# Kernel optimization log

Measured on AMD Instinct MI355X. Metric: run time of the kernel, lower is better.

## Reference

```python
import jax, jax.numpy as jnp
import numpy as np

B, S, E = 2, 2048, 1024
H = 16
A = 1024
DH = A // H  # 64 per-head attention dim


def setup_inputs() -> dict:
    key = jax.random.key(0)
    ks = jax.random.split(key, 9)
    s = lambda fan_in: 1.0 / np.sqrt(fan_in)
    return {
        "x": jax.random.normal(ks[0], (B, S, E), dtype=jnp.float32),
        # per-head Q/K/V projections stacked over heads: [H, E, DH]
        "Wq": jax.random.normal(ks[1], (H, E, DH), dtype=jnp.float32) * s(E),
        "bq": jnp.zeros((H, DH), dtype=jnp.float32),
        "Wk": jax.random.normal(ks[2], (H, E, DH), dtype=jnp.float32) * s(E),
        "bk": jnp.zeros((H, DH), dtype=jnp.float32),
        "Wv": jax.random.normal(ks[3], (H, E, DH), dtype=jnp.float32) * s(E),
        "bv": jnp.zeros((H, DH), dtype=jnp.float32),
        # output projection Linear(A, E): stored as [A, E]
        "Wo": jax.random.normal(ks[4], (A, E), dtype=jnp.float32) * s(A),
        "bo": jnp.zeros((E,), dtype=jnp.float32),
    }


def reference(x, Wq, bq, Wk, bk, Wv, bv, Wo, bo):
    # Batched equivalent of the per-head Python loop:
    # each head: q = x Wq_h + bq_h ; scores = q k^T / sqrt(DH) ; softmax ; @ v
    q = jnp.einsum("bse,hed->bhsd", x, Wq) + bq[None, :, None, :]
    k = jnp.einsum("bse,hed->bhsd", x, Wk) + bk[None, :, None, :]
    v = jnp.einsum("bse,hed->bhsd", x, Wv) + bv[None, :, None, :]
    scale = 1.0 / jnp.sqrt(jnp.asarray(DH, dtype=x.dtype))
    scores = jnp.einsum("bhsd,bhtd->bhst", q, k) * scale  # [B,H,S,S]
    attn = jax.nn.softmax(scores, axis=-1)
    heads = jnp.einsum("bhst,bhtd->bhsd", attn, v)  # [B,H,S,DH]
    # concat heads along last dim (matches torch.cat over head outputs)
    concat = heads.transpose(0, 2, 1, 3).reshape(x.shape[0], x.shape[1], H * DH)
    return concat @ Wo + bo  # final Linear(dim_attention, dim_embedding)
```

## Files before the change

kernel.cpp:

```cpp
#include <hip/hip_runtime.h>
#include <math.h>


namespace {
constexpr int kBn = 2, kS = 2048, kE = 1024, kH = 16, kDH = 64, kA = 1024;

typedef __attribute__((ext_vector_type(8))) short short8;
typedef __attribute__((ext_vector_type(4))) float f32x4;

#define QSCALE 0.18033688011112042f

__device__ inline unsigned short f2bf(float f) {
  union { float f; unsigned u; } x; x.f = f;
  unsigned r = x.u + 0x7fffu + ((x.u >> 16) & 1u);
  return (unsigned short)(r >> 16);
}

__device__ inline void gld16(const void* g, void* l) {
  __builtin_amdgcn_global_load_lds(
      (const __attribute__((address_space(1))) unsigned int*)g,
      (__attribute__((address_space(3))) unsigned int*)l, 16, 0, 0);
}

__global__ __launch_bounds__(256) void cast_x_kernel(
    const float* __restrict__ x, unsigned short* __restrict__ xb) {
  const int i = (blockIdx.x * 256 + threadIdx.x) * 8;
  float4 a = *(const float4*)(x + i);
  float4 b = *(const float4*)(x + i + 4);
  unsigned short t[8];
  t[0] = f2bf(a.x); t[1] = f2bf(a.y); t[2] = f2bf(a.z); t[3] = f2bf(a.w);
  t[4] = f2bf(b.x); t[5] = f2bf(b.y); t[6] = f2bf(b.z); t[7] = f2bf(b.w);
  *(short8*)(xb + i) = *(const short8*)t;
}

__global__ __launch_bounds__(256) void cast_wqkv_kernel(
    const float* __restrict__ Wq, const float* __restrict__ Wk,
    const float* __restrict__ Wv, unsigned short* __restrict__ Wt) {
  const int sel = blockIdx.z;
  const float* __restrict__ W = (sel == 0) ? Wq : (sel == 1) ? Wk : Wv;
  const int h = blockIdx.y;
  const int e0 = blockIdx.x * 64;
  const int tid = threadIdx.x;

  __shared__ float T[64][68];
  const int el = tid >> 2, dq = tid & 3;
  const float* src = W + ((size_t)h * kE + e0 + el) * kDH + dq * 16;
#pragma unroll
  for (int j = 0; j < 4; ++j)
    *(float4*)&T[el][dq * 16 + j * 4] = *(const float4*)(src + j * 4);
  __syncthreads();

  const int d = tid & 63, w = tid >> 6;
  unsigned short t[16];
#pragma unroll
  for (int j = 0; j < 16; ++j) t[j] = f2bf(T[w * 16 + j][d]);
  unsigned short* dst =
      Wt + (((size_t)sel << 20) | ((size_t)(h * 64 + d) << 10)) + e0 + w * 16;
  *(short8*)dst = *(const short8*)&t[0];
  *(short8*)(dst + 8) = *(const short8*)&t[8];
}

__global__ __launch_bounds__(256) void cast_wo_kernel(
    const float* __restrict__ Wo, unsigned short* __restrict__ Wot) {
  const int a0 = blockIdx.x * 64, e0 = blockIdx.y * 64;
  const int tid = threadIdx.x;

  __shared__ float T[64][68];
  const int al = tid >> 2, dq = tid & 3;
  const float* src = Wo + (size_t)(a0 + al) * kE + e0 + dq * 16;
#pragma unroll
  for (int j = 0; j < 4; ++j)
    *(float4*)&T[al][dq * 16 + j * 4] = *(const float4*)(src + j * 4);
  __syncthreads();

  const int e = tid & 63, w = tid >> 6;
  unsigned short t[16];
#pragma unroll
  for (int j = 0; j < 16; ++j) t[j] = f2bf(T[w * 16 + j][e]);
  unsigned short* dst = Wot + ((size_t)(e0 + e) << 10) + a0 + w * 16;
  *(short8*)dst = *(const short8*)&t[0];
  *(short8*)(dst + 8) = *(const short8*)&t[8];
}

__global__ __launch_bounds__(256) void gemm_bf16_kernel(
    const unsigned short* __restrict__ A, const unsigned short* __restrict__ Bt,
    const float* __restrict__ b0, const float* __restrict__ b1,
    const float* __restrict__ b2,
    unsigned short* __restrict__ oq, unsigned short* __restrict__ okk,
    unsigned short* __restrict__ ov, float* __restrict__ of, int modeBase) {
  constexpr int K = 1024;
  const int mode = modeBase ? 3 : (int)blockIdx.z;
  const unsigned short* Bm = Bt + ((size_t)(modeBase ? 0 : blockIdx.z) << 20);
  const float* bias = (mode == 1) ? b1 : (mode == 2) ? b2 : b0;

  const int mt = blockIdx.x, nt = blockIdx.y;
  const int tid = threadIdx.x;
  const int wv = tid >> 6, lane = tid & 63, lq = lane & 15, quad = lane >> 4;
  const int wm = wv >> 1, wn = wv & 1;

  __shared__ unsigned short lA[128 * 32];
  __shared__ unsigned short lB[128 * 32];

  const int c0 = wv * 64 + lane;
  const int c1 = c0 + 256;
  const unsigned short* gA0 = A + (size_t)(mt * 128 + (c0 >> 2)) * K + (c0 & 3) * 8;
  const unsigned short* gA1 = A + (size_t)(mt * 128 + (c1 >> 2)) * K + (c1 & 3) * 8;
  const unsigned short* gB0 = Bm + (size_t)(nt * 128 + (c0 >> 2)) * K + (c0 & 3) * 8;
  const unsigned short* gB1 = Bm + (size_t)(nt * 128 + (c1 >> 2)) * K + (c1 & 3) * 8;
  unsigned short* lA0 = lA + (size_t)(wv * 64) * 8;
  unsigned short* lA1 = lA0 + 256 * 8;
  unsigned short* lB0 = lB + (size_t)(wv * 64) * 8;
  unsigned short* lB1 = lB0 + 256 * 8;

  f32x4 acc[4][4];
#pragma unroll
  for (int i = 0; i < 4; ++i)
#pragma unroll
    for (int j = 0; j < 4; ++j) acc[i][j] = (f32x4){0.f, 0.f, 0.f, 0.f};

  for (int k0 = 0; k0 < K; k0 += 32) {
    gld16(gA0 + k0, lA0);
    gld16(gA1 + k0, lA1);
    gld16(gB0 + k0, lB0);
    gld16(gB1 + k0, lB1);
    __syncthreads();
    short8 af[4], bfr[4];
#pragma unroll
    for (int i = 0; i < 4; ++i)
      af[i] = *(const short8*)&lA[(wm * 64 + i * 16 + lq) * 32 + quad * 8];
#pragma unroll
    for (int j = 0; j < 4; ++j)
      bfr[j] = *(const short8*)&lB[(wn * 64 + j * 16 + lq) * 32 + quad * 8];
#pragma unroll
    for (int i = 0; i < 4; ++i)
#pragma unroll
      for (int j = 0; j < 4; ++j)
        acc[i][j] = __builtin_amdgcn_mfma_f32_16x16x32_bf16(af[i], bfr[j],
                                                            acc[i][j], 0, 0, 0);
    __syncthreads();
  }

  const int n0 = nt * 128 + wn * 64;
  float bv4[4];
#pragma unroll
  for (int j = 0; j < 4; ++j) bv4[j] = bias[n0 + j * 16 + lq];

  if (mode == 3) {
    const int m0 = mt * 128 + wm * 64;
#pragma unroll
    for (int i = 0; i < 4; ++i)
#pragma unroll
      for (int j = 0; j < 4; ++j)
#pragma unroll
        for (int r = 0; r < 4; ++r)
          of[(size_t)(m0 + i * 16 + quad * 4 + r) * kE + n0 + j * 16 + lq] =
              acc[i][j][r] + bv4[j];
  } else {
    const int tok0 = mt * 128 + wm * 64;
    const int b = tok0 >> 11;
    const int s0 = tok0 & (kS - 1);
    const int h = n0 >> 6;
    if (mode < 2) {
      unsigned short* o = (mode == 0) ? oq : okk;
      const float scl = (mode == 0) ? QSCALE : 1.0f;
#pragma unroll
      for (int i = 0; i < 4; ++i)
#pragma unroll
        for (int j = 0; j < 4; ++j) {
          const int d = j * 16 + lq;
#pragma unroll
          for (int r = 0; r < 4; ++r) {
            const int s = s0 + i * 16 + quad * 4 + r;
            o[((size_t)(b * kH + h) * kS + s) * kDH + d] =
                f2bf((acc[i][j][r] + bv4[j]) * scl);
          }
        }
    } else {
#pragma unroll
      for (int i = 0; i < 4; ++i)
#pragma unroll
        for (int j = 0; j < 4; ++j) {
          const int d = j * 16 + lq;
          union { unsigned short u[4]; uint2 v; } pk;
#pragma unroll
          for (int r = 0; r < 4; ++r) pk.u[r] = f2bf(acc[i][j][r] + bv4[j]);
          const int s = s0 + i * 16 + quad * 4;
          *(uint2*)(ov + ((size_t)(b * kH + h) * kDH + d) * kS + s) = pk.v;
        }
    }
  }
}

#define QT 64
#define KT 64
#define LDK 72
__global__ __launch_bounds__(256) void attn_mfma_kernel(
    const unsigned short* __restrict__ q, const unsigned short* __restrict__ k,
    const unsigned short* __restrict__ vt, unsigned short* __restrict__ cc) {
  const int bh = blockIdx.y;
  const int b = bh >> 4, h = bh & 15;
  const int tid = threadIdx.x;
  const int wv = tid >> 6;
  const int lane = tid & 63;
  const int lq = lane & 15;
  const int quad = lane >> 4;

  __shared__ unsigned short Ks[KT][LDK];
  __shared__ unsigned short Vt[kDH][LDK];
  __shared__ unsigned short Pb[QT][LDK];

  const int q0 = blockIdx.x * QT;

  const unsigned short* qbase = q + ((size_t)bh * kS + q0 + wv * 16 + lq) * kDH;
  const short8 qa0 = *(const short8*)(qbase + quad * 8);
  const short8 qa1 = *(const short8*)(qbase + 32 + quad * 8);

  f32x4 Oacc[4];
#pragma unroll
  for (int dt = 0; dt < 4; ++dt) Oacc[dt] = (f32x4){0.f, 0.f, 0.f, 0.f};
  f32x4 Osum = (f32x4){0.f, 0.f, 0.f, 0.f};

  unsigned short ob[8];
#pragma unroll
  for (int i = 0; i < 8; ++i) ob[i] = 0x3F80;
  const short8 ones = *(const short8*)ob;

  const unsigned short* kg = k + (size_t)bh * kS * kDH;
  const unsigned short* vg = vt + (size_t)bh * kDH * kS;

  for (int t0 = 0; t0 < kS; t0 += KT) {
    __syncthreads();
#pragma unroll
    for (int p = 0; p < 2; ++p) {
      const int id = p * 256 + tid;
      const int row = id >> 3, c = (id & 7) << 3;
      *(short8*)&Ks[row][c] = *(const short8*)(kg + (size_t)(t0 + row) * kDH + c);
      *(short8*)&Vt[row][c] = *(const short8*)(vg + (size_t)row * kS + t0 + c);
    }
    __syncthreads();

    f32x4 S[4];
#pragma unroll
    for (int nt = 0; nt < 4; ++nt) {
      short8 b0 = *(const short8*)&Ks[nt * 16 + lq][quad * 8];
      short8 b1 = *(const short8*)&Ks[nt * 16 + lq][32 + quad * 8];
      f32x4 acc = (f32x4){0.f, 0.f, 0.f, 0.f};
      acc = __builtin_amdgcn_mfma_f32_16x16x32_bf16(qa0, b0, acc, 0, 0, 0);
      acc = __builtin_amdgcn_mfma_f32_16x16x32_bf16(qa1, b1, acc, 0, 0, 0);
      S[nt] = acc;
    }

#pragma unroll
    for (int nt = 0; nt < 4; ++nt)
#pragma unroll
      for (int r = 0; r < 4; ++r) {
        const float p = __builtin_amdgcn_exp2f(S[nt][r]);
        union { float f; unsigned u; } x; x.f = p;
        Pb[wv * 16 + quad * 4 + r][nt * 16 + lq] =
            (unsigned short)((x.u + 0x8000u) >> 16);
      }

    const short8 pa0 = *(const short8*)&Pb[wv * 16 + lq][quad * 8];
    const short8 pa1 = *(const short8*)&Pb[wv * 16 + lq][32 + quad * 8];
#pragma unroll
    for (int dt = 0; dt < 4; ++dt) {
      short8 vb0 = *(const short8*)&Vt[dt * 16 + lq][quad * 8];
      short8 vb1 = *(const short8*)&Vt[dt * 16 + lq][32 + quad * 8];
      Oacc[dt] = __builtin_amdgcn_mfma_f32_16x16x32_bf16(pa0, vb0, Oacc[dt], 0, 0, 0);
      Oacc[dt] = __builtin_amdgcn_mfma_f32_16x16x32_bf16(pa1, vb1, Oacc[dt], 0, 0, 0);
    }
    Osum = __builtin_amdgcn_mfma_f32_16x16x32_bf16(pa0, ones, Osum, 0, 0, 0);
    Osum = __builtin_amdgcn_mfma_f32_16x16x32_bf16(pa1, ones, Osum, 0, 0, 0);
  }

#pragma unroll
  for (int r = 0; r < 4; ++r) {
    const float inv = 1.0f / Osum[r];
    const int qrow = q0 + wv * 16 + quad * 4 + r;
    unsigned short* base = cc + ((size_t)b * kS + qrow) * kA + h * kDH;
#pragma unroll
    for (int dt = 0; dt < 4; ++dt) base[dt * 16 + lq] = f2bf(Oacc[dt][r] * inv);
  }
}

}

extern "C" void kernel_launch(void* const* d_in, const int* in_sizes, int n_in,
                              void* d_out, int out_size, void* d_ws, size_t ws_size,
                              hipStream_t stream) {
  const float* x  = (const float*)d_in[0];
  const float* Wq = (const float*)d_in[1];
  const float* bq = (const float*)d_in[2];
  const float* Wk = (const float*)d_in[3];
  const float* bk = (const float*)d_in[4];
  const float* Wv = (const float*)d_in[5];
  const float* bv = (const float*)d_in[6];
  const float* Wo = (const float*)d_in[7];
  const float* bo = (const float*)d_in[8];
  float* out = (float*)d_out;

  const size_t per = (size_t)kBn * kH * kS * kDH;
  unsigned short* xb  = (unsigned short*)d_ws;
  unsigned short* qb  = xb + per;
  unsigned short* kb  = qb + per;
  unsigned short* vtb = kb + per;
  unsigned short* cc  = vtb + per;
  unsigned short* Wt  = cc + per;
  unsigned short* Wot = Wt + 3 * (per / 4);

  cast_x_kernel<<<dim3(per / (256 * 8)), 256, 0, stream>>>(x, xb);
  cast_wqkv_kernel<<<dim3(16, 16, 3), 256, 0, stream>>>(Wq, Wk, Wv, Wt);
  cast_wo_kernel<<<dim3(16, 16), 256, 0, stream>>>(Wo, Wot);

  gemm_bf16_kernel<<<dim3(32, 8, 3), 256, 0, stream>>>(
      xb, Wt, bq, bk, bv, qb, kb, vtb, nullptr, 0);

  attn_mfma_kernel<<<dim3(kS / QT, kBn * kH), 256, 0, stream>>>(qb, kb, vtb, cc);

  gemm_bf16_kernel<<<dim3(32, 8, 1), 256, 0, stream>>>(
      cc, Wot, bo, nullptr, nullptr, nullptr, nullptr, nullptr, out, 1);
}
```

Baseline: 218.2 us.

## Prefetch K/V tiles into registers in attention and add narrower output GEMM

After: 209.2 us. -4.1%, faster.

```diff
diff --git a/kernel.cpp b/kernel.cpp
--- a/kernel.cpp
+++ b/kernel.cpp
@@ -20,6 +20,11 @@
   __builtin_amdgcn_global_load_lds(
       (const __attribute__((address_space(1))) unsigned int*)g,
       (__attribute__((address_space(3))) unsigned int*)l, 16, 0, 0);
+}
+
+__device__ inline void lds_barrier() {
+  asm volatile("s_waitcnt lgkmcnt(0)" ::: "memory");
+  __builtin_amdgcn_s_barrier();
 }
 
 __global__ __launch_bounds__(256) void cast_x_kernel(
@@ -87,10 +92,10 @@
     const float* __restrict__ b0, const float* __restrict__ b1,
     const float* __restrict__ b2,
     unsigned short* __restrict__ oq, unsigned short* __restrict__ okk,
-    unsigned short* __restrict__ ov, float* __restrict__ of, int modeBase) {
+    unsigned short* __restrict__ ov) {
   constexpr int K = 1024;
-  const int mode = modeBase ? 3 : (int)blockIdx.z;
-  const unsigned short* Bm = Bt + ((size_t)(modeBase ? 0 : blockIdx.z) << 20);
+  const int mode = (int)blockIdx.z;
+  const unsigned short* Bm = Bt + ((size_t)blockIdx.z << 20);
   const float* bias = (mode == 1) ? b1 : (mode == 2) ? b2 : b0;
 
   const int mt = blockIdx.x, nt = blockIdx.y;
@@ -145,50 +150,101 @@
 #pragma unroll
   for (int j = 0; j < 4; ++j) bv4[j] = bias[n0 + j * 16 + lq];
 
-  if (mode == 3) {
-    const int m0 = mt * 128 + wm * 64;
-#pragma unroll
-    for (int i = 0; i < 4; ++i)
-#pragma unroll
-      for (int j = 0; j < 4; ++j)
-#pragma unroll
-        for (int r = 0; r < 4; ++r)
-          of[(size_t)(m0 + i * 16 + quad * 4 + r) * kE + n0 + j * 16 + lq] =
-              acc[i][j][r] + bv4[j];
+  const int tok0 = mt * 128 + wm * 64;
+  const int b = tok0 >> 11;
+  const int s0 = tok0 & (kS - 1);
+  const int h = n0 >> 6;
+  if (mode < 2) {
+    unsigned short* o = (mode == 0) ? oq : okk;
+    const float scl = (mode == 0) ? QSCALE : 1.0f;
+#pragma unroll
+    for (int i = 0; i < 4; ++i)
+#pragma unroll
+      for (int j = 0; j < 4; ++j) {
+        const int d = j * 16 + lq;
+#pragma unroll
+        for (int r = 0; r < 4; ++r) {
+          const int s = s0 + i * 16 + quad * 4 + r;
+          o[((size_t)(b * kH + h) * kS + s) * kDH + d] =
+              f2bf((acc[i][j][r] + bv4[j]) * scl);
+        }
+      }
   } else {
-    const int tok0 = mt * 128 + wm * 64;
-    const int b = tok0 >> 11;
-    const int s0 = tok0 & (kS - 1);
-    const int h = n0 >> 6;
-    if (mode < 2) {
-      unsigned short* o = (mode == 0) ? oq : okk;
-      const float scl = (mode == 0) ? QSCALE : 1.0f;
-#pragma unroll
-      for (int i = 0; i < 4; ++i)
-#pragma unroll
-        for (int j = 0; j < 4; ++j) {
-          const int d = j * 16 + lq;
-#pragma unroll
-          for (int r = 0; r < 4; ++r) {
-            const int s = s0 + i * 16 + quad * 4 + r;
-            o[((size_t)(b * kH + h) * kS + s) * kDH + d] =
-                f2bf((acc[i][j][r] + bv4[j]) * scl);
-          }
-        }
-    } else {
-#pragma unroll
-      for (int i = 0; i < 4; ++i)
-#pragma unroll
-        for (int j = 0; j < 4; ++j) {
-          const int d = j * 16 + lq;
-          union { unsigned short u[4]; uint2 v; } pk;
-#pragma unroll
-          for (int r = 0; r < 4; ++r) pk.u[r] = f2bf(acc[i][j][r] + bv4[j]);
-          const int s = s0 + i * 16 + quad * 4;
-          *(uint2*)(ov + ((size_t)(b * kH + h) * kDH + d) * kS + s) = pk.v;
-        }
-    }
-  }
+#pragma unroll
+    for (int i = 0; i < 4; ++i)
+#pragma unroll
+      for (int j = 0; j < 4; ++j) {
+        const int d = j * 16 + lq;
+        union { unsigned short u[4]; uint2 v; } pk;
+#pragma unroll
+        for (int r = 0; r < 4; ++r) pk.u[r] = f2bf(acc[i][j][r] + bv4[j]);
+        const int s = s0 + i * 16 + quad * 4;
+        *(uint2*)(ov + ((size_t)(b * kH + h) * kDH + d) * kS + s) = pk.v;
+      }
+  }
+}
+
+__global__ __launch_bounds__(256) void gemm_out_kernel(
+    const unsigned short* __restrict__ A, const unsigned short* __restrict__ Bt,
+    const float* __restrict__ bo, float* __restrict__ of) {
+  constexpr int K = 1024;
+  const int mt = blockIdx.x, nt = blockIdx.y;
+  const int tid = threadIdx.x;
+  const int wv = tid >> 6, lane = tid & 63, lq = lane & 15, quad = lane >> 4;
+  const int wm = wv >> 1, wn = wv & 1;
+
+  __shared__ unsigned short lA[128 * 32];
+  __shared__ unsigned short lB[64 * 32];
+
+  const int c0 = wv * 64 + lane;
+  const int c1 = c0 + 256;
+  const unsigned short* gA0 = A + (size_t)(mt * 128 + (c0 >> 2)) * K + (c0 & 3) * 8;
+  const unsigned short* gA1 = A + (size_t)(mt * 128 + (c1 >> 2)) * K + (c1 & 3) * 8;
+  const unsigned short* gB0 = Bt + (size_t)(nt * 64 + (c0 >> 2)) * K + (c0 & 3) * 8;
+  unsigned short* lA0 = lA + (size_t)(wv * 64) * 8;
+  unsigned short* lA1 = lA0 + 256 * 8;
+  unsigned short* lB0 = lB + (size_t)(wv * 64) * 8;
+
+  f32x4 acc[4][2];
+#pragma unroll
+  for (int i = 0; i < 4; ++i)
+#pragma unroll
+    for (int j = 0; j < 2; ++j) acc[i][j] = (f32x4){0.f, 0.f, 0.f, 0.f};
+
+  for (int k0 = 0; k0 < K; k0 += 32) {
+    gld16(gA0 + k0, lA0);
+    gld16(gA1 + k0, lA1);
+    gld16(gB0 + k0, lB0);
+    __syncthreads();
+    short8 af[4], bfr[2];
+#pragma unroll
+    for (int i = 0; i < 4; ++i)
+      af[i] = *(const short8*)&lA[(wm * 64 + i * 16 + lq) * 32 + quad * 8];
+#pragma unroll
+    for (int j = 0; j < 2; ++j)
+      bfr[j] = *(const short8*)&lB[(wn * 32 + j * 16 + lq) * 32 + quad * 8];
+#pragma unroll
+    for (int i = 0; i < 4; ++i)
+#pragma unroll
+      for (int j = 0; j < 2; ++j)
+        acc[i][j] = __builtin_amdgcn_mfma_f32_16x16x32_bf16(af[i], bfr[j],
+                                                            acc[i][j], 0, 0, 0);
+    __syncthreads();
+  }
+
+  const int n0 = nt * 64 + wn * 32;
+  const int m0 = mt * 128 + wm * 64;
+  float bv2[2];
+#pragma unroll
+  for (int j = 0; j < 2; ++j) bv2[j] = bo[n0 + j * 16 + lq];
+#pragma unroll
+  for (int i = 0; i < 4; ++i)
+#pragma unroll
+    for (int j = 0; j < 2; ++j)
+#pragma unroll
+      for (int r = 0; r < 4; ++r)
+        of[(size_t)(m0 + i * 16 + quad * 4 + r) * kE + n0 + j * 16 + lq] =
+            acc[i][j][r] + bv2[j];
 }
 
 #define QT 64
@@ -228,16 +284,28 @@
   const unsigned short* kg = k + (size_t)bh * kS * kDH;
   const unsigned short* vg = vt + (size_t)bh * kDH * kS;
 
+  const int sr = tid >> 3;
+  const int sc = (tid & 7) << 3;
+
+  short8 rk0 = *(const short8*)(kg + (size_t)sr * kDH + sc);
+  short8 rk1 = *(const short8*)(kg + (size_t)(sr + 32) * kDH + sc);
+  short8 rv0 = *(const short8*)(vg + (size_t)sr * kS + sc);
+  short8 rv1 = *(const short8*)(vg + (size_t)(sr + 32) * kS + sc);
+
   for (int t0 = 0; t0 < kS; t0 += KT) {
-    __syncthreads();
-#pragma unroll
-    for (int p = 0; p < 2; ++p) {
-      const int id = p * 256 + tid;
-      const int row = id >> 3, c = (id & 7) << 3;
-      *(short8*)&Ks[row][c] = *(const short8*)(kg + (size_t)(t0 + row) * kDH + c);
-      *(short8*)&Vt[row][c] = *(const short8*)(vg + (size_t)row * kS + t0 + c);
+    lds_barrier();
+    *(short8*)&Ks[sr][sc]       = rk0;
+    *(short8*)&Ks[sr + 32][sc]  = rk1;
+    *(short8*)&Vt[sr][sc]       = rv0;
+    *(short8*)&Vt[sr + 32][sc]  = rv1;
+    if (t0 + KT < kS) {
+      const int tn = t0 + KT;
+      rk0 = *(const short8*)(kg + (size_t)(tn + sr) * kDH + sc);
+      rk1 = *(const short8*)(kg + (size_t)(tn + sr + 32) * kDH + sc);
+      rv0 = *(const short8*)(vg + (size_t)sr * kS + tn + sc);
+      rv1 = *(const short8*)(vg + (size_t)(sr + 32) * kS + tn + sc);
     }
-    __syncthreads();
+    lds_barrier();
 
     f32x4 S[4];
 #pragma unroll
@@ -313,10 +381,9 @@
   cast_wo_kernel<<<dim3(16, 16), 256, 0, stream>>>(Wo, Wot);
 
   gemm_bf16_kernel<<<dim3(32, 8, 3), 256, 0, stream>>>(
-      xb, Wt, bq, bk, bv, qb, kb, vtb, nullptr, 0);
+      xb, Wt, bq, bk, bv, qb, kb, vtb);
 
   attn_mfma_kernel<<<dim3(kS / QT, kBn * kH), 256, 0, stream>>>(qb, kb, vtb, cc);
 
-  gemm_bf16_kernel<<<dim3(32, 8, 1), 256, 0, stream>>>(
-      cc, Wot, bo, nullptr, nullptr, nullptr, nullptr, nullptr, out, 1);
-}
+  gemm_out_kernel<<<dim3(32, 16), 256, 0, stream>>>(cc, Wot, bo, out);
+}
```
